# Kernel tuning notes

Measured on AMD Instinct MI355X. Metric: run time of the kernel, lower is better.

## Reference

```python
import jax, jax.numpy as jnp
import numpy as np

B, S, D, E, R = 8, 4096, 768, 8, 8

def setup_inputs() -> dict:
    key = jax.random.key(0)
    ks = jax.random.split(key, 9)
    sc = 0.02
    return {
        "x":  jax.random.normal(ks[0], (B, S, D), dtype=jnp.float32),
        "Wd": jax.random.normal(ks[1], (E, D, R), dtype=jnp.float32) * sc,
        "bd": jax.random.normal(ks[2], (E, R), dtype=jnp.float32) * sc,
        "Wm": jax.random.normal(ks[3], (E, R, R), dtype=jnp.float32) * sc,
        "bm": jax.random.normal(ks[4], (E, R), dtype=jnp.float32) * sc,
        "Wu": jax.random.normal(ks[5], (E, R, D), dtype=jnp.float32) * sc,
        "bu": jax.random.normal(ks[6], (E, D), dtype=jnp.float32) * sc,
        "Wg": jax.random.normal(ks[7], (D, E), dtype=jnp.float32) * sc,
        "bg": jax.random.normal(ks[8], (E,), dtype=jnp.float32) * sc,
    }

def reference(x, Wd, bd, Wm, bm, Wu, bu, Wg, bg):
    # Gating: softmax over experts. [B,S,E]
    gate = jax.nn.softmax(jnp.einsum('bsd,de->bse', x, Wg) + bg, axis=-1)
    # All experts batched as 3D GEMMs (dropout = identity, eval mode).
    h = jnp.einsum('bsd,edr->bser', x, Wd) + bd            # [B,S,E,R] down
    h = jnp.einsum('bser,erq->bseq', h, Wm) + bm           # [B,S,E,R] mid
    up = jnp.einsum('bser,erd->bsed', h, Wu) + bu          # [B,S,E,D] up
    # Weighted sum over experts.
    return jnp.einsum('bse,bsed->bsd', gate, up)
```

## Files before the change

kernel.cpp:

```cpp
#include <hip/hip_runtime.h>
#include <stdint.h>


typedef short bf16x8 __attribute__((ext_vector_type(8)));
typedef float f32x4 __attribute__((ext_vector_type(4)));

static __device__ __forceinline__ unsigned short f2bf(float f) {
  union { float f; uint32_t u; } v; v.f = f;
  return (unsigned short)((v.u + 0x7fffu + ((v.u >> 16) & 1u)) >> 16);
}

__global__ void prep_weights(const float* __restrict__ Wd, const float* __restrict__ Wg,
                             const float* __restrict__ Wu, const float* __restrict__ bu,
                             unsigned short* __restrict__ w1f, unsigned short* __restrict__ w2f) {
  int tid = blockIdx.x * 256 + threadIdx.x;
  const int N1 = 24 * 5 * 64 * 8;
  if (tid < N1) {
    int i    = tid & 7;
    int lane = (tid >> 3) & 63;
    int fk   = tid >> 9;
    int f = fk % 5, K0 = fk / 5;
    int k = K0 * 32 + (lane >> 4) * 8 + i;
    int j = f * 16 + (lane & 15);
    float val = 0.f;
    if (j < 64)      val = Wd[(size_t)(j >> 3) * 6144 + (size_t)k * 8 + (j & 7)];
    else if (j < 72) val = Wg[(size_t)k * 8 + (j - 64)];
    w1f[tid] = f2bf(val);
  } else {
    int t2 = tid - N1;
    if (t2 >= 48 * 3 * 64 * 8) return;
    int i    = t2 & 7;
    int lane = (t2 >> 3) & 63;
    int tk   = t2 >> 9;
    int K0 = tk % 3, T = tk / 3;
    int k = K0 * 32 + (lane >> 4) * 8 + i;
    int n = T * 16 + (lane & 15);
    float val = 0.f;
    if (k < 64)      val = Wu[(size_t)(k >> 3) * 6144 + (size_t)(k & 7) * 768 + n];
    else if (k < 72) val = bu[(size_t)(k - 64) * 768 + n];
    w2f[t2] = f2bf(val);
  }
}

__global__ __launch_bounds__(256) void k1_g2(
    const float* __restrict__ x,
    const float* __restrict__ bd, const float* __restrict__ Wm,
    const float* __restrict__ bm, const float* __restrict__ bg,
    const unsigned short* __restrict__ w1f, unsigned int* __restrict__ g2) {
  __shared__ float Hs[2][32][84];

  const int tidx = threadIdx.x;
  const int lane = tidx & 63;
  const int wave = tidx >> 6;
  const int tg   = wave >> 1;
  const int kh   = wave & 1;
  const int arow = lane & 15;
  const int kgrp = lane >> 4;
  const int tok0 = blockIdx.x * 32;

  {
    const float* xrow = x + (size_t)(tok0 + tg * 16 + arow) * 768 + kh * 384 + kgrp * 8;
    f32x4 acc0 = {0,0,0,0}, acc1 = {0,0,0,0}, acc2 = {0,0,0,0}, acc3 = {0,0,0,0}, acc4 = {0,0,0,0};
    const bf16x8* w1v = (const bf16x8*)w1f + (size_t)(kh * 12) * 320 + lane;

    float4 xa[4][2];
    #pragma unroll
    for (int i = 0; i < 4; i++) {
      xa[i][0] = *(const float4*)(xrow + i * 32);
      xa[i][1] = *(const float4*)(xrow + i * 32 + 4);
    }
    #pragma unroll
    for (int i = 0; i < 12; i++) {
      float4 a0 = xa[i & 3][0];
      float4 a1 = xa[i & 3][1];
      if (i + 4 < 12) {
        xa[i & 3][0] = *(const float4*)(xrow + (i + 4) * 32);
        xa[i & 3][1] = *(const float4*)(xrow + (i + 4) * 32 + 4);
      }
      bf16x8 af;
      af[0] = (short)f2bf(a0.x); af[1] = (short)f2bf(a0.y);
      af[2] = (short)f2bf(a0.z); af[3] = (short)f2bf(a0.w);
      af[4] = (short)f2bf(a1.x); af[5] = (short)f2bf(a1.y);
      af[6] = (short)f2bf(a1.z); af[7] = (short)f2bf(a1.w);
      const bf16x8* bb = w1v + i * 320;
      acc0 = __builtin_amdgcn_mfma_f32_16x16x32_bf16(af, bb[0],   acc0, 0, 0, 0);
      acc1 = __builtin_amdgcn_mfma_f32_16x16x32_bf16(af, bb[64],  acc1, 0, 0, 0);
      acc2 = __builtin_amdgcn_mfma_f32_16x16x32_bf16(af, bb[128], acc2, 0, 0, 0);
      acc3 = __builtin_amdgcn_mfma_f32_16x16x32_bf16(af, bb[192], acc3, 0, 0, 0);
      acc4 = __builtin_amdgcn_mfma_f32_16x16x32_bf16(af, bb[256], acc4, 0, 0, 0);
    }
    int hr = tg * 16 + kgrp * 4;
    #pragma unroll
    for (int r = 0; r < 4; r++) {
      Hs[kh][hr + r][arow]      = acc0[r];
      Hs[kh][hr + r][16 + arow] = acc1[r];
      Hs[kh][hr + r][32 + arow] = acc2[r];
      Hs[kh][hr + r][48 + arow] = acc3[r];
      Hs[kh][hr + r][64 + arow] = acc4[r];
    }
  }
  __syncthreads();

  if (tidx < 128) {
    int t = tidx >> 2;
    int c = tidx & 3;
    unsigned int* g2u = g2 + (size_t)(tok0 + t) * 48;
    float lg[8];
    float m = -1e30f;
    #pragma unroll
    for (int e = 0; e < 8; e++) {
      lg[e] = Hs[0][t][64 + e] + Hs[1][t][64 + e] + bg[e];
      m = fmaxf(m, lg[e]);
    }
    float den = 0.f;
    #pragma unroll
    for (int e = 0; e < 8; e++) { lg[e] = __expf(lg[e] - m); den += lg[e]; }
    float inv = 1.f / den;
    unsigned int hv[8];
    #pragma unroll
    for (int ee = 0; ee < 2; ee++) {
      int e = c * 2 + ee;
      float gate = lg[e] * inv;
      float h[8];
      #pragma unroll
      for (int r = 0; r < 8; r++)
        h[r] = Hs[0][t][e * 8 + r] + Hs[1][t][e * 8 + r] + bd[e * 8 + r];
      #pragma unroll
      for (int q = 0; q < 8; q += 2) {
        float h2a = bm[e * 8 + q], h2b = bm[e * 8 + q + 1];
        #pragma unroll
        for (int r = 0; r < 8; r++) {
          h2a += h[r] * Wm[e * 64 + r * 8 + q];
          h2b += h[r] * Wm[e * 64 + r * 8 + q + 1];
        }
        hv[ee * 4 + (q >> 1)] =
            (unsigned)f2bf(gate * h2a) | ((unsigned)f2bf(gate * h2b) << 16);
      }
    }
    *(uint4*)(g2u + 8 * c)     = make_uint4(hv[0], hv[1], hv[2], hv[3]);
    *(uint4*)(g2u + 8 * c + 4) = make_uint4(hv[4], hv[5], hv[6], hv[7]);
    g2u[32 + c] = (unsigned)f2bf(lg[c * 2] * inv) | ((unsigned)f2bf(lg[c * 2 + 1] * inv) << 16);
    g2u[36 + c * 3 + 0] = 0;
    g2u[36 + c * 3 + 1] = 0;
    g2u[36 + c * 3 + 2] = 0;
  }
}

__global__ __launch_bounds__(256) void k2_out(
    const unsigned short* __restrict__ g2bf, const unsigned short* __restrict__ w2f,
    float* __restrict__ out) {
  const int tidx = threadIdx.x;
  const int lane = tidx & 63;
  const int wave = tidx >> 6;
  const int arow = lane & 15;
  const int kgrp = lane >> 4;
  const int tok0 = blockIdx.x * 32;

  const unsigned short* grow0 = g2bf + (size_t)(tok0 + arow) * 96 + kgrp * 8;
  const unsigned short* grow1 = grow0 + 16 * 96;
  bf16x8 a0_0 = *(const bf16x8*)(grow0);
  bf16x8 a0_1 = *(const bf16x8*)(grow0 + 32);
  bf16x8 a0_2 = *(const bf16x8*)(grow0 + 64);
  bf16x8 a1_0 = *(const bf16x8*)(grow1);
  bf16x8 a1_1 = *(const bf16x8*)(grow1 + 32);
  bf16x8 a1_2 = *(const bf16x8*)(grow1 + 64);

  const bf16x8* w2v = (const bf16x8*)w2f + (size_t)(wave * 12) * 192 + lane;
  float* orow0 = out + (size_t)(tok0 + arow) * 768 + wave * 192 + kgrp * 4;
  float* orow1 = orow0 + (size_t)16 * 768;

  bf16x8 pb[4][3];
  #pragma unroll
  for (int d = 0; d < 4; d++) {
    pb[d][0] = w2v[d * 192];
    pb[d][1] = w2v[d * 192 + 64];
    pb[d][2] = w2v[d * 192 + 128];
  }
  #pragma unroll
  for (int j = 0; j < 12; j++) {
    bf16x8 b0 = pb[j & 3][0], b1 = pb[j & 3][1], b2 = pb[j & 3][2];
    if (j + 4 < 12) {
      pb[j & 3][0] = w2v[(j + 4) * 192];
      pb[j & 3][1] = w2v[(j + 4) * 192 + 64];
      pb[j & 3][2] = w2v[(j + 4) * 192 + 128];
    }
    f32x4 c0 = {0,0,0,0}, c1 = {0,0,0,0};
    c0 = __builtin_amdgcn_mfma_f32_16x16x32_bf16(b0, a0_0, c0, 0, 0, 0);
    c1 = __builtin_amdgcn_mfma_f32_16x16x32_bf16(b0, a1_0, c1, 0, 0, 0);
    c0 = __builtin_amdgcn_mfma_f32_16x16x32_bf16(b1, a0_1, c0, 0, 0, 0);
    c1 = __builtin_amdgcn_mfma_f32_16x16x32_bf16(b1, a1_1, c1, 0, 0, 0);
    c0 = __builtin_amdgcn_mfma_f32_16x16x32_bf16(b2, a0_2, c0, 0, 0, 0);
    c1 = __builtin_amdgcn_mfma_f32_16x16x32_bf16(b2, a1_2, c1, 0, 0, 0);
    *(f32x4*)(orow0 + j * 16) = c0;
    *(f32x4*)(orow1 + j * 16) = c1;
  }
}

extern "C" void kernel_launch(void* const* d_in, const int* in_sizes, int n_in,
                              void* d_out, int out_size, void* d_ws, size_t ws_size,
                              hipStream_t stream) {
  const float* x  = (const float*)d_in[0];
  const float* Wd = (const float*)d_in[1];
  const float* bd = (const float*)d_in[2];
  const float* Wm = (const float*)d_in[3];
  const float* bm = (const float*)d_in[4];
  const float* Wu = (const float*)d_in[5];
  const float* bu = (const float*)d_in[6];
  const float* Wg = (const float*)d_in[7];
  const float* bg = (const float*)d_in[8];
  unsigned short* w1f = (unsigned short*)d_ws;
  unsigned short* w2f = w1f + 61440;
  unsigned int*   g2  = (unsigned int*)((char*)d_ws + 270336);

  prep_weights<<<528, 256, 0, stream>>>(Wd, Wg, Wu, bu, w1f, w2f);
  k1_g2<<<1024, 256, 0, stream>>>(x, bd, Wm, bm, bg, w1f, g2);
  k2_out<<<1024, 256, 0, stream>>>((const unsigned short*)g2, w2f, (float*)d_out);
}
```

Before: 61.66 us.

## Interleave down-projection and up-projection blocks across staggered launches

Merges the two main kernels into a single role-dispatched kernel and launches it five times, so each launch runs k1 blocks for one chunk of tokens alongside k2 blocks for the previous chunk. The aim is to mix the input-read-heavy stage with the output-write-heavy stage on the device at the same time, rather than running them as two separate phases. It also shrinks the w2 prefetch depth from 4 to 2 stages to save registers. In exchange it adds more kernel launches, and the merged kernel's register use is set by the larger of the two bodies, which can lower occupancy for the lighter role.

```diff
diff --git a/kernel.cpp b/kernel.cpp
--- a/kernel.cpp
+++ b/kernel.cpp
@@ -42,8 +42,8 @@
   }
 }
 
-__global__ __launch_bounds__(256) void k1_g2(
-    const float* __restrict__ x,
+__device__ __forceinline__ void k1_body(
+    int tok0, const float* __restrict__ x,
     const float* __restrict__ bd, const float* __restrict__ Wm,
     const float* __restrict__ bm, const float* __restrict__ bg,
     const unsigned short* __restrict__ w1f, unsigned int* __restrict__ g2) {
@@ -56,7 +56,6 @@
   const int kh   = wave & 1;
   const int arow = lane & 15;
   const int kgrp = lane >> 4;
-  const int tok0 = blockIdx.x * 32;
 
   {
     const float* xrow = x + (size_t)(tok0 + tg * 16 + arow) * 768 + kh * 384 + kgrp * 8;
@@ -146,15 +145,14 @@
   }
 }
 
-__global__ __launch_bounds__(256) void k2_out(
-    const unsigned short* __restrict__ g2bf, const unsigned short* __restrict__ w2f,
-    float* __restrict__ out) {
+__device__ __forceinline__ void k2_body(
+    int tok0, const unsigned short* __restrict__ g2bf,
+    const unsigned short* __restrict__ w2f, float* __restrict__ out) {
   const int tidx = threadIdx.x;
   const int lane = tidx & 63;
   const int wave = tidx >> 6;
   const int arow = lane & 15;
   const int kgrp = lane >> 4;
-  const int tok0 = blockIdx.x * 32;
 
   const unsigned short* grow0 = g2bf + (size_t)(tok0 + arow) * 96 + kgrp * 8;
   const unsigned short* grow1 = grow0 + 16 * 96;
@@ -169,20 +167,20 @@
   float* orow0 = out + (size_t)(tok0 + arow) * 768 + wave * 192 + kgrp * 4;
   float* orow1 = orow0 + (size_t)16 * 768;
 
-  bf16x8 pb[4][3];
+  bf16x8 pb[2][3];
   #pragma unroll
-  for (int d = 0; d < 4; d++) {
+  for (int d = 0; d < 2; d++) {
     pb[d][0] = w2v[d * 192];
     pb[d][1] = w2v[d * 192 + 64];
     pb[d][2] = w2v[d * 192 + 128];
   }
   #pragma unroll
   for (int j = 0; j < 12; j++) {
-    bf16x8 b0 = pb[j & 3][0], b1 = pb[j & 3][1], b2 = pb[j & 3][2];
-    if (j + 4 < 12) {
-      pb[j & 3][0] = w2v[(j + 4) * 192];
-      pb[j & 3][1] = w2v[(j + 4) * 192 + 64];
-      pb[j & 3][2] = w2v[(j + 4) * 192 + 128];
+    bf16x8 b0 = pb[j & 1][0], b1 = pb[j & 1][1], b2 = pb[j & 1][2];
+    if (j + 2 < 12) {
+      pb[j & 1][0] = w2v[(j + 2) * 192];
+      pb[j & 1][1] = w2v[(j + 2) * 192 + 64];
+      pb[j & 1][2] = w2v[(j + 2) * 192 + 128];
     }
     f32x4 c0 = {0,0,0,0}, c1 = {0,0,0,0};
     c0 = __builtin_amdgcn_mfma_f32_16x16x32_bf16(b0, a0_0, c0, 0, 0, 0);
@@ -193,6 +191,28 @@
     c1 = __builtin_amdgcn_mfma_f32_16x16x32_bf16(b2, a1_2, c1, 0, 0, 0);
     *(f32x4*)(orow0 + j * 16) = c0;
     *(f32x4*)(orow1 + j * 16) = c1;
+  }
+}
+
+__global__ __launch_bounds__(256) void moba_roles(
+    const float* __restrict__ x,
+    const float* __restrict__ bd, const float* __restrict__ Wm,
+    const float* __restrict__ bm, const float* __restrict__ bg,
+    const unsigned short* __restrict__ w1f, const unsigned short* __restrict__ w2f,
+    unsigned int* __restrict__ g2, float* __restrict__ out,
+    int k1_base, int k1_n, int k2_base, int k2_n) {
+  const int bid = blockIdx.x;
+  int role, idx;
+  if (k2_n == 0)      { role = 0; idx = bid; }
+  else if (k1_n == 0) { role = 1; idx = bid; }
+  else {
+    role = (bid >> 3) & 1;
+    idx  = ((bid >> 4) << 3) + (bid & 7);
+  }
+  if (role == 0) {
+    k1_body((k1_base + idx) * 32, x, bd, Wm, bm, bg, w1f, g2);
+  } else {
+    k2_body((k2_base + idx) * 32, (const unsigned short*)g2, w2f, out);
   }
 }
 
@@ -211,8 +231,17 @@
   unsigned short* w1f = (unsigned short*)d_ws;
   unsigned short* w2f = w1f + 61440;
   unsigned int*   g2  = (unsigned int*)((char*)d_ws + 270336);
+  float* out = (float*)d_out;
 
   prep_weights<<<528, 256, 0, stream>>>(Wd, Wg, Wu, bu, w1f, w2f);
-  k1_g2<<<1024, 256, 0, stream>>>(x, bd, Wm, bm, bg, w1f, g2);
-  k2_out<<<1024, 256, 0, stream>>>((const unsigned short*)g2, w2f, (float*)d_out);
-}
+  moba_roles<<<256, 256, 0, stream>>>(x, bd, Wm, bm, bg, w1f, w2f, g2, out,
+                                      0, 256, 0, 0);
+  moba_roles<<<512, 256, 0, stream>>>(x, bd, Wm, bm, bg, w1f, w2f, g2, out,
+                                      256, 256, 0, 256);
+  moba_roles<<<512, 256, 0, stream>>>(x, bd, Wm, bm, bg, w1f, w2f, g2, out,
+                                      512, 256, 256, 256);
+  moba_roles<<<512, 256, 0, stream>>>(x, bd, Wm, bm, bg, w1f, w2f, g2, out,
+                                      768, 256, 512, 256);
+  moba_roles<<<256, 256, 0, stream>>>(x, bd, Wm, bm, bg, w1f, w2f, g2, out,
+                                      0, 0, 768, 256);
+}
```

After: 77.71 us. +26.0%, slower.
